# Kernel optimization log

Measured on AMD Instinct MI355X. Metric: run time of the kernel, lower is better.

The kernel has to match this reference:

```python
import jax, jax.numpy as jnp
import numpy as np

SEQ, H, VOCAB = 2048, 1024, 32000

def setup_inputs() -> dict:
    key = jax.random.key(0)
    ks = jax.random.split(key, 13)
    s = lambda k, shape, fan: jax.random.normal(k, shape, dtype=jnp.float32) / np.sqrt(fan)
    return {
        "word_input": jax.random.randint(ks[0], (1,), 0, VOCAB, dtype=jnp.int64),
        "last_context": s(ks[1], (1, H), H),
        "last_hidden": s(ks[2], (1, H), H),
        "encoder_outputs": s(ks[3], (SEQ, H), H),
        "emb": s(ks[4], (VOCAB, H), H),
        "W_ih": s(ks[5], (4 * H, 2 * H), 2 * H),
        "W_hh": s(ks[6], (4 * H, H), H),
        "b_ih": s(ks[7], (4 * H,), H),
        "b_hh": s(ks[8], (4 * H,), H),
        "Wa": s(ks[9], (H, H), H),
        "ba": s(ks[10], (H,), H),
        "Wl": s(ks[11], (VOCAB, 2 * H), 2 * H),
        "bl": s(ks[12], (VOCAB,), 2 * H),
    }

def reference(word_input, last_context, last_hidden, encoder_outputs,
              emb, W_ih, W_hh, b_ih, b_hh, Wa, ba, Wl, bl):
    # embedding lookup (batch=1, single step): [H]
    x = emb[word_input[0]]
    # rnn_input = cat(embedded, last_context): [2H]
    inp = jnp.concatenate([x, last_context[0]])
    h0 = last_hidden[0]
    c0 = jnp.zeros_like(h0)
    # single LSTM step, PyTorch gate order (i, f, g, o)
    gates = W_ih @ inp + b_ih + W_hh @ h0 + b_hh  # [4H]
    i_g, f_g, g_g, o_g = jnp.split(gates, 4)
    c = jax.nn.sigmoid(f_g) * c0 + jax.nn.sigmoid(i_g) * jnp.tanh(g_g)
    h = jax.nn.sigmoid(o_g) * jnp.tanh(c)  # lstm_output, [H]
    # Bahdanau-style scores: dot(h, Wa @ enc_i + ba) for each position (vectorized)
    energies = (encoder_outputs @ Wa.T + ba) @ h  # [SEQ]
    attn_w = jax.nn.softmax(energies)
    context = attn_w @ encoder_outputs  # [H]
    logits = Wl @ jnp.concatenate([h, context]) + bl  # [VOCAB]
    out = jax.nn.log_softmax(logits)
    return out[None, :]  # [1, VOCAB]
```

## Files before the change

### kernel.cpp

```cpp
#include <hip/hip_runtime.h>
#include <hip/hip_bf16.h>
#include <math.h>

#define SEQ   2048
#define H     1024
#define VOCAB 32000
#define GRID2 2048
#define NTHR  256

__device__ inline float4 ld4(const float* p) { return *reinterpret_cast<const float4*>(p); }
__device__ inline float dot4(float4 a, float4 b) { return a.x*b.x + a.y*b.y + a.z*b.z + a.w*b.w; }
__device__ inline float sigmoidf(float x) { return 1.f / (1.f + expf(-x)); }

__device__ inline void omerge(float& m, float& s, float m2, float s2) {
    if (m2 > m) { s = s * __expf(m - m2) + s2; m = m2; }
    else if (s2 != 0.f) { s += s2 * __expf(m2 - m); }
}
__device__ inline float waveSum(float v) {
#pragma unroll
    for (int off = 32; off > 0; off >>= 1) v += __shfl_down(v, off, 64);
    return v;
}
__device__ inline void waveOmerge(float& m, float& s) {
#pragma unroll
    for (int off = 32; off > 0; off >>= 1) {
        float m2 = __shfl_down(m, off, 64), ss = __shfl_down(s, off, 64);
        omerge(m, s, m2, ss);
    }
}

__device__ inline void blockSignal(unsigned* f) {
    __syncthreads();
    if (threadIdx.x == 0) {
        __threadfence();
        __hip_atomic_fetch_add(f, 1u, __ATOMIC_RELEASE, __HIP_MEMORY_SCOPE_AGENT);
    }
}
__device__ inline void blockWait(unsigned* f, unsigned target) {
    if (threadIdx.x == 0) {
        while (__hip_atomic_load(f, __ATOMIC_ACQUIRE, __HIP_MEMORY_SCOPE_AGENT) < target)
            __builtin_amdgcn_s_sleep(4);
        __threadfence();
    }
    __syncthreads();
}


__global__ __launch_bounds__(NTHR) void k_init(float* __restrict__ ws) {
    const int t = threadIdx.x;
    unsigned* fl = (unsigned*)ws;
    if (t < 96) fl[t] = 0u;
    float* u   = ws + 2144;
    float* ctx = ws + 1120;
    for (int k = t; k < H; k += NTHR) { u[k] = 0.f; ctx[k] = 0.f; }
}

__global__ __launch_bounds__(NTHR, 8) void k_main(
        const float* __restrict__ emb,  const float* __restrict__ lctx,
        const float* __restrict__ h0,   const float* __restrict__ W_ih,
        const float* __restrict__ W_hh, const float* __restrict__ b_ih,
        const float* __restrict__ b_hh, const int* __restrict__ widx,
        const float* __restrict__ enc,  const float* __restrict__ Wa,
        const float* __restrict__ Wl,   const float* __restrict__ bl,
        float* __restrict__ ws, float* __restrict__ out) {
    const int bid = blockIdx.x, t = threadIdx.x;
    const int wid = t >> 6, lane = t & 63;

    unsigned* f_h   = (unsigned*)ws + 0;
    unsigned* f_u   = (unsigned*)ws + 16;
    unsigned* f_e   = (unsigned*)ws + 32;
    unsigned* f_ctx = (unsigned*)ws + 48;
    unsigned* f_l   = (unsigned*)ws + 64;
    float*  h      = ws + 96;
    float*  ctx    = ws + 1120;
    float*  u      = ws + 2144;
    float*  energ  = ws + 3168;
    float2* part_e = (float2*)(ws + 5216);
    float2* part_l = (float2*)(ws + 5728);

    __shared__ float  lg[12];
    __shared__ float  shh[16];
    __shared__ float  se[8];
    __shared__ float  shw[32];
    __shared__ float2 s2[4];

    if (bid >= 1024) {
        const int j = bid - 1024;
        const int w = widx[0];
        const float* xe = emb + (size_t)w * H;
        const float* wi = W_ih + (size_t)j * (2 * H);
        const float* wg = W_ih + (size_t)(j + 2 * H) * (2 * H);
        const float* wo = W_ih + (size_t)(j + 3 * H) * (2 * H);
        const float* vi = W_hh + (size_t)j * H;
        const float* vg = W_hh + (size_t)(j + 2 * H) * H;
        const float* vo = W_hh + (size_t)(j + 3 * H) * H;
        const int e = t * 4;
        float4 x0 = ld4(xe + e), x1 = ld4(lctx + e), x2 = ld4(h0 + e);
        float ai = dot4(ld4(wi + e), x0) + dot4(ld4(wi + H + e), x1) + dot4(ld4(vi + e), x2);
        float ag = dot4(ld4(wg + e), x0) + dot4(ld4(wg + H + e), x1) + dot4(ld4(vg + e), x2);
        float ao = dot4(ld4(wo + e), x0) + dot4(ld4(wo + H + e), x1) + dot4(ld4(vo + e), x2);
        ai = waveSum(ai); ag = waveSum(ag); ao = waveSum(ao);
        if (lane == 0) { lg[wid*3] = ai; lg[wid*3+1] = ag; lg[wid*3+2] = ao; }
        __syncthreads();
        if (t == 0) {
            float gi = 0.f, gg = 0.f, go = 0.f;
            for (int q = 0; q < 4; ++q) { gi += lg[q*3]; gg += lg[q*3+1]; go += lg[q*3+2]; }
            gi += b_ih[j] + b_hh[j];
            gg += b_ih[j + 2*H] + b_hh[j + 2*H];
            go += b_ih[j + 3*H] + b_hh[j + 3*H];
            float c = sigmoidf(gi) * tanhf(gg);
            h[j] = sigmoidf(go) * tanhf(c);
        }
        blockSignal(f_h);
    }

    blockWait(f_h, 1024);

    if (bid < 256) {
        {
            const int rg = bid >> 2, kb = bid & 3;
            if (t < 16) shh[t] = h[rg * 16 + t];
            __syncthreads();
            const int k = kb * 256 + t;
            float acc = 0.f;
#pragma unroll
            for (int jj = 0; jj < 16; ++jj)
                acc += Wa[(size_t)(rg * 16 + jj) * H + k] * shh[jj];
            atomicAdd(&u[k], acc);
            blockSignal(f_u);
            blockWait(f_u, 256);
        }
        {
#pragma unroll
            for (int rr = 0; rr < 2; ++rr) {
                const int row = bid * 8 + wid * 2 + rr;
                const float* er = enc + (size_t)row * H;
                float acc = 0.f;
#pragma unroll
                for (int it = 0; it < 4; ++it) {
                    const int e = it * 256 + lane * 4;
                    acc += dot4(ld4(er + e), ld4(u + e));
                }
                acc = waveSum(acc);
                if (lane == 0) { energ[row] = acc; se[wid * 2 + rr] = acc; }
            }
            __syncthreads();
            if (t == 0) {
                float m = -INFINITY, s = 0.f;
                for (int q = 0; q < 8; ++q) omerge(m, s, se[q], 1.f);
                part_e[bid] = make_float2(m, s);
            }
            blockSignal(f_e);
            blockWait(f_e, 256);
        }
        {
            float2 p = part_e[t];
            float m = p.x, s = p.y;
            waveOmerge(m, s);
            if (lane == 0) s2[wid] = make_float2(m, s);
            __syncthreads();
            float M = s2[0].x, S = s2[0].y;
#pragma unroll
            for (int q = 1; q < 4; ++q) omerge(M, S, s2[q].x, s2[q].y);
            const float invS = 1.f / S;
            const int rg = bid >> 2, kb = bid & 3;
            __syncthreads();
            if (t < 32) shw[t] = __expf(energ[rg * 32 + t] - M) * invS;
            __syncthreads();
            const int k = kb * 256 + t;
            float acc = 0.f;
#pragma unroll
            for (int jj = 0; jj < 32; ++jj)
                acc += shw[jj] * enc[(size_t)(rg * 32 + jj) * H + k];
            atomicAdd(&ctx[k], acc);
            blockSignal(f_ctx);
        }
        if (bid < 125) {
            blockWait(f_l, 1792);
            float m = -INFINITY, s = 0.f;
            for (int i = t; i < 1792; i += NTHR) {
                float2 p = part_l[i];
                omerge(m, s, p.x, p.y);
            }
            waveOmerge(m, s);
            __syncthreads();
            if (lane == 0) s2[wid] = make_float2(m, s);
            __syncthreads();
            float M = s2[0].x, S = s2[0].y;
#pragma unroll
            for (int q = 1; q < 4; ++q) omerge(M, S, s2[q].x, s2[q].y);
            const float lse = M + logf(S);
            const int i = bid * 256 + t;
            out[i] = out[i] - lse;
        }
    } else {
        const int gwS = (bid - 256) * 4 + wid;
        const int NR = (gwS < 3328) ? 5 : 4;
        float4 xv[4];
#pragma unroll
        for (int q = 0; q < 4; ++q) xv[q] = ld4(h + q * 256 + lane * 4);
        float acc[5] = {0.f, 0.f, 0.f, 0.f, 0.f};
#pragma unroll
        for (int rr = 0; rr < 5; ++rr) {
            if (rr < NR) {
                const float* wr = Wl + (size_t)(gwS + 7168 * rr) * (2 * H);
                float a = 0.f;
#pragma unroll
                for (int q = 0; q < 4; ++q)
                    a += dot4(ld4(wr + q * 256 + lane * 4), xv[q]);
                acc[rr] = a;
            }
        }
        blockWait(f_ctx, 256);
#pragma unroll
        for (int q = 0; q < 4; ++q) xv[q] = ld4(ctx + q * 256 + lane * 4);
        float lm = -INFINITY, ls = 0.f;
#pragma unroll
        for (int rr = 0; rr < 5; ++rr) {
            if (rr < NR) {
                const int r = gwS + 7168 * rr;
                const float* wr = Wl + (size_t)r * (2 * H) + H;
                float a = acc[rr];
#pragma unroll
                for (int q = 0; q < 4; ++q)
                    a += dot4(ld4(wr + q * 256 + lane * 4), xv[q]);
                a = waveSum(a);
                if (lane == 0) {
                    float v = a + bl[r];
                    out[r] = v;
                    omerge(lm, ls, v, 1.f);
                }
            }
        }
        if (lane == 0) s2[wid] = make_float2(lm, ls);
        __syncthreads();
        if (t == 0) {
            float M = s2[0].x, S = s2[0].y;
#pragma unroll
            for (int q = 1; q < 4; ++q) omerge(M, S, s2[q].x, s2[q].y);
            part_l[bid - 256] = make_float2(M, S);
        }
        blockSignal(f_l);
    }
}


__global__ __launch_bounds__(256) void k_lstm(
        const float* __restrict__ emb, const float* __restrict__ lctx,
        const float* __restrict__ h0,  const float* __restrict__ W_ih,
        const float* __restrict__ W_hh, const float* __restrict__ b_ih,
        const float* __restrict__ b_hh, const int* __restrict__ widx,
        float* __restrict__ h_out, float* __restrict__ u_zero,
        float* __restrict__ ctx_zero) {
    const int j = blockIdx.x, t = threadIdx.x;
    const int wid = t >> 6, lane = t & 63;
    if (j == 0) for (int k = t; k < H; k += 256) u_zero[k] = 0.f;
    if (j == 1) for (int k = t; k < H; k += 256) ctx_zero[k] = 0.f;
    const int w = widx[0];
    const float* embrow = emb + (size_t)w * H;
    const int ri = j, rg = j + 2 * H, ro = j + 3 * H;
    const float* wi_i = W_ih + (size_t)ri * (2 * H);
    const float* wi_g = W_ih + (size_t)rg * (2 * H);
    const float* wi_o = W_ih + (size_t)ro * (2 * H);
    const float* wh_i = W_hh + (size_t)ri * H;
    const float* wh_g = W_hh + (size_t)rg * H;
    const float* wh_o = W_hh + (size_t)ro * H;
    float ai = 0.f, ag = 0.f, ao = 0.f;
    { int e = t*4; float4 x = ld4(embrow+e);
      ai += dot4(ld4(wi_i+e),x); ag += dot4(ld4(wi_g+e),x); ao += dot4(ld4(wi_o+e),x); }
    { int e = t*4; float4 x = ld4(lctx+e);
      ai += dot4(ld4(wi_i+H+e),x); ag += dot4(ld4(wi_g+H+e),x); ao += dot4(ld4(wi_o+H+e),x); }
    { int e = t*4; float4 x = ld4(h0+e);
      ai += dot4(ld4(wh_i+e),x); ag += dot4(ld4(wh_g+e),x); ao += dot4(ld4(wh_o+e),x); }
    ai = waveSum(ai); ag = waveSum(ag); ao = waveSum(ao);
    __shared__ float lds[12];
    if (lane == 0) { lds[wid*3] = ai; lds[wid*3+1] = ag; lds[wid*3+2] = ao; }
    __syncthreads();
    if (t == 0) {
        float gi = 0.f, gg = 0.f, go = 0.f;
        for (int q = 0; q < 4; ++q) { gi += lds[q*3]; gg += lds[q*3+1]; go += lds[q*3+2]; }
        gi += b_ih[ri] + b_hh[ri];
        gg += b_ih[rg] + b_hh[rg];
        go += b_ih[ro] + b_hh[ro];
        float c = sigmoidf(gi) * tanhf(gg);
        h_out[j] = sigmoidf(go) * tanhf(c);
    }
}

__global__ __launch_bounds__(256) void k_wa(
        const float* __restrict__ Wa, const float* __restrict__ h,
        float* __restrict__ u) {
    const int k = blockIdx.x * 256 + threadIdx.x;
    const int j0 = blockIdx.y * 32;
    float acc = 0.f;
#pragma unroll 8
    for (int j = j0; j < j0 + 32; ++j) acc += Wa[(size_t)j * H + k] * h[j];
    atomicAdd(&u[k], acc);
}

__global__ __launch_bounds__(256) void k_energy(
        const float* __restrict__ enc, const float* __restrict__ u,
        float* __restrict__ energ, float2* __restrict__ part_e) {
    const int t = threadIdx.x, wid = t >> 6, lane = t & 63;
    const int row = blockIdx.x * 4 + wid;
    const float* er = enc + (size_t)row * H;
    float acc = 0.f;
#pragma unroll
    for (int it = 0; it < 4; ++it) { int e = it*256 + lane*4; acc += dot4(ld4(er+e), ld4(u+e)); }
    acc = waveSum(acc);
    __shared__ float se[4];
    if (lane == 0) { energ[row] = acc; se[wid] = acc; }
    __syncthreads();
    if (t == 0) {
        float m = fmaxf(fmaxf(se[0], se[1]), fmaxf(se[2], se[3]));
        float s = __expf(se[0]-m) + __expf(se[1]-m) + __expf(se[2]-m) + __expf(se[3]-m);
        part_e[blockIdx.x] = make_float2(m, s);
    }
}

__global__ __launch_bounds__(256) void k_ctx(
        const float* __restrict__ enc, const float* __restrict__ energ,
        const float2* __restrict__ part_e, float* __restrict__ ctx) {
    const int t = threadIdx.x, wid = t >> 6, lane = t & 63;
    __shared__ float2 s2[4];
    __shared__ float sh[64];
    float2 a = part_e[t], b = part_e[t + 256];
    float m = a.x, s = a.y;
    omerge(m, s, b.x, b.y);
    waveOmerge(m, s);
    if (lane == 0) s2[wid] = make_float2(m, s);
    __syncthreads();
    float M = s2[0].x, S = s2[0].y;
#pragma unroll
    for (int q = 1; q < 4; ++q) omerge(M, S, s2[q].x, s2[q].y);
    const float invS = 1.f / S;
    const int j0 = (blockIdx.x >> 2) * 64;
    __syncthreads();
    if (t < 64) sh[t] = __expf(energ[j0 + t] - M) * invS;
    __syncthreads();
    const int k = (blockIdx.x & 3) * 256 + t;
    float acc = 0.f;
#pragma unroll 8
    for (int jj = 0; jj < 64; ++jj) acc += sh[jj] * enc[(size_t)(j0 + jj) * H + k];
    atomicAdd(&ctx[k], acc);
}

__global__ __launch_bounds__(256) void k_logits(
        const float* __restrict__ Wl, const float* __restrict__ vcat,
        const float* __restrict__ bl, float* __restrict__ logits,
        float2* __restrict__ part_l) {
    const int t = threadIdx.x, wid = t >> 6, lane = t & 63;
    const int gw = blockIdx.x * 4 + wid;
    float4 xv[8];
#pragma unroll
    for (int q = 0; q < 8; ++q) xv[q] = ld4(vcat + q * 256 + lane * 4);
    float lm = -INFINITY, ls = 0.f;
#pragma unroll
    for (int rr = 0; rr < 4; ++rr) {
        const int row = gw * 4 + rr;
        const float* wr = Wl + (size_t)row * (2 * H);
        float acc = 0.f;
#pragma unroll
        for (int q = 0; q < 8; ++q)
            acc += dot4(ld4(wr + q * 256 + lane * 4), xv[q]);
        acc = waveSum(acc);
        if (lane == 0) {
            float v = acc + bl[row];
            logits[row] = v;
            omerge(lm, ls, v, 1.f);
        }
    }
    __shared__ float2 s2[4];
    if (lane == 0) s2[wid] = make_float2(lm, ls);
    __syncthreads();
    if (t == 0) {
        float M = s2[0].x, S = s2[0].y;
#pragma unroll
        for (int q = 1; q < 4; ++q) omerge(M, S, s2[q].x, s2[q].y);
        part_l[blockIdx.x] = make_float2(M, S);
    }
}

__global__ __launch_bounds__(256) void k_final(
        const float* __restrict__ logits, const float2* __restrict__ part_l,
        float* __restrict__ out) {
    const int t = threadIdx.x, wid = t >> 6, lane = t & 63;
    __shared__ float2 s2[4];
    float m = -INFINITY, s = 0.f;
    for (int i = t; i < 2000; i += 256) {
        float2 p = part_l[i];
        omerge(m, s, p.x, p.y);
    }
    waveOmerge(m, s);
    if (lane == 0) s2[wid] = make_float2(m, s);
    __syncthreads();
    float M = s2[0].x, S = s2[0].y;
#pragma unroll
    for (int q = 1; q < 4; ++q) omerge(M, S, s2[q].x, s2[q].y);
    const float lse = M + logf(S);
    const int i = blockIdx.x * 256 + t;
    out[i] = logits[i] - lse;
}

extern "C" void kernel_launch(void* const* d_in, const int* in_sizes, int n_in,
                              void* d_out, int out_size, void* d_ws, size_t ws_size,
                              hipStream_t stream) {
    const int*   widx = (const int*)d_in[0];
    const float* lctx = (const float*)d_in[1];
    const float* h0   = (const float*)d_in[2];
    const float* enc  = (const float*)d_in[3];
    const float* emb  = (const float*)d_in[4];
    const float* W_ih = (const float*)d_in[5];
    const float* W_hh = (const float*)d_in[6];
    const float* b_ih = (const float*)d_in[7];
    const float* b_hh = (const float*)d_in[8];
    const float* Wa   = (const float*)d_in[9];
    const float* Wl   = (const float*)d_in[11];
    const float* bl   = (const float*)d_in[12];
    float* out = (float*)d_out;
    float* ws  = (float*)d_ws;

    int occ = 0, nCU = 0, dev = 0;
    hipGetDevice(&dev);
    hipDeviceGetAttribute(&nCU, hipDeviceAttributeMultiprocessorCount, dev);
    hipError_t oe = hipOccupancyMaxActiveBlocksPerMultiprocessor(
        &occ, (const void*)k_main, NTHR, 0);
    const bool persistent_ok = (oe == hipSuccess) && ((long)occ * nCU >= GRID2);

    if (persistent_ok) {
        k_init<<<1, NTHR, 0, stream>>>(ws);
        k_main<<<GRID2, NTHR, 0, stream>>>(emb, lctx, h0, W_ih, W_hh, b_ih,
                                           b_hh, widx, enc, Wa, Wl, bl, ws, out);
    } else {
        float*  h      = ws;
        float*  ctx    = ws + 1024;
        float*  u      = ws + 2048;
        float*  energ  = ws + 3072;
        float2* part_e = (float2*)(ws + 5120);
        float2* part_l = (float2*)(ws + 6144);
        float*  logits = ws + 10240;
        k_lstm  <<<1024, 256, 0, stream>>>(emb, lctx, h0, W_ih, W_hh, b_ih, b_hh, widx, h, u, ctx);
        k_wa    <<<dim3(4, 32), 256, 0, stream>>>(Wa, h, u);
        k_energy<<<512, 256, 0, stream>>>(enc, u, energ, part_e);
        k_ctx   <<<128, 256, 0, stream>>>(enc, energ, part_e, ctx);
        k_logits<<<2000, 256, 0, stream>>>(Wl, ws , bl, logits, part_l);
        k_final <<<125, 256, 0, stream>>>(logits, part_l, out);
    }
}
```

Baseline: 72.98 us.

## Rebalance fused decoder blocks: LSTM blocks also do logits, attention blocks take tail rows

```diff
diff --git a/kernel.cpp b/kernel.cpp
--- a/kernel.cpp
+++ b/kernel.cpp
@@ -9,6 +9,11 @@
 #define NTHR  256
 
 __device__ inline float4 ld4(const float* p) { return *reinterpret_cast<const float4*>(p); }
+typedef float vfloat4 __attribute__((ext_vector_type(4)));
+__device__ inline float4 ld4nt(const float* p) {
+    vfloat4 v = __builtin_nontemporal_load(reinterpret_cast<const vfloat4*>(p));
+    return make_float4(v.x, v.y, v.z, v.w);
+}
 __device__ inline float dot4(float4 a, float4 b) { return a.x*b.x + a.y*b.y + a.z*b.z + a.w*b.w; }
 __device__ inline float sigmoidf(float x) { return 1.f / (1.f + expf(-x)); }
 
@@ -49,9 +54,9 @@
 __global__ __launch_bounds__(NTHR) void k_init(float* __restrict__ ws) {
     const int t = threadIdx.x;
     unsigned* fl = (unsigned*)ws;
-    if (t < 96) fl[t] = 0u;
-    float* u   = ws + 2144;
-    float* ctx = ws + 1120;
+    if (t < 128) fl[t] = 0u;
+    float* ctx = ws + 1152;
+    float* u   = ws + 2176;
     for (int k = t; k < H; k += NTHR) { u[k] = 0.f; ctx[k] = 0.f; }
 }
 
@@ -71,12 +76,13 @@
     unsigned* f_e   = (unsigned*)ws + 32;
     unsigned* f_ctx = (unsigned*)ws + 48;
     unsigned* f_l   = (unsigned*)ws + 64;
-    float*  h      = ws + 96;
-    float*  ctx    = ws + 1120;
-    float*  u      = ws + 2144;
-    float*  energ  = ws + 3168;
-    float2* part_e = (float2*)(ws + 5216);
-    float2* part_l = (float2*)(ws + 5728);
+    float*  vcat   = ws + 128;
+    float*  h      = vcat;
+    float*  ctx    = vcat + H;
+    float*  u      = ws + 2176;
+    float*  energ  = ws + 3200;
+    float2* part_e = (float2*)(ws + 5248);
+    float2* part_l = (float2*)(ws + 5760);
 
     __shared__ float  lg[12];
     __shared__ float  shh[16];
@@ -84,10 +90,10 @@
     __shared__ float  shw[32];
     __shared__ float2 s2[4];
 
-    if (bid >= 1024) {
-        const int j = bid - 1024;
+    if (bid < 1024) {
+        const int j = bid;
         const int w = widx[0];
-        const float* xe = emb + (size_t)w * H;
+        const float* xep = emb + (size_t)w * H;
         const float* wi = W_ih + (size_t)j * (2 * H);
         const float* wg = W_ih + (size_t)(j + 2 * H) * (2 * H);
         const float* wo = W_ih + (size_t)(j + 3 * H) * (2 * H);
@@ -95,10 +101,10 @@
         const float* vg = W_hh + (size_t)(j + 2 * H) * H;
         const float* vo = W_hh + (size_t)(j + 3 * H) * H;
         const int e = t * 4;
-        float4 x0 = ld4(xe + e), x1 = ld4(lctx + e), x2 = ld4(h0 + e);
-        float ai = dot4(ld4(wi + e), x0) + dot4(ld4(wi + H + e), x1) + dot4(ld4(vi + e), x2);
-        float ag = dot4(ld4(wg + e), x0) + dot4(ld4(wg + H + e), x1) + dot4(ld4(vg + e), x2);
-        float ao = dot4(ld4(wo + e), x0) + dot4(ld4(wo + H + e), x1) + dot4(ld4(vo + e), x2);
+        float4 x0 = ld4(xep + e), x1 = ld4(lctx + e), x2 = ld4(h0 + e);
+        float ai = dot4(ld4nt(wi + e), x0) + dot4(ld4nt(wi + H + e), x1) + dot4(ld4nt(vi + e), x2);
+        float ag = dot4(ld4nt(wg + e), x0) + dot4(ld4nt(wg + H + e), x1) + dot4(ld4nt(vg + e), x2);
+        float ao = dot4(ld4nt(wo + e), x0) + dot4(ld4nt(wo + H + e), x1) + dot4(ld4nt(vo + e), x2);
         ai = waveSum(ai); ag = waveSum(ag); ao = waveSum(ao);
         if (lane == 0) { lg[wid*3] = ai; lg[wid*3+1] = ag; lg[wid*3+2] = ao; }
         __syncthreads();
@@ -116,9 +122,10 @@
 
     blockWait(f_h, 1024);
 
-    if (bid < 256) {
+    if (bid >= 1024 && bid < 1280) {
+        const int ab = bid - 1024;
         {
-            const int rg = bid >> 2, kb = bid & 3;
+            const int rg = ab >> 2, kb = ab & 3;
             if (t < 16) shh[t] = h[rg * 16 + t];
             __syncthreads();
             const int k = kb * 256 + t;
@@ -133,7 +140,7 @@
         {
 #pragma unroll
             for (int rr = 0; rr < 2; ++rr) {
-                const int row = bid * 8 + wid * 2 + rr;
+                const int row = ab * 8 + wid * 2 + rr;
                 const float* er = enc + (size_t)row * H;
                 float acc = 0.f;
 #pragma unroll
@@ -148,7 +155,7 @@
             if (t == 0) {
                 float m = -INFINITY, s = 0.f;
                 for (int q = 0; q < 8; ++q) omerge(m, s, se[q], 1.f);
-                part_e[bid] = make_float2(m, s);
+                part_e[ab] = make_float2(m, s);
             }
             blockSignal(f_e);
             blockWait(f_e, 256);
@@ -163,7 +170,7 @@
 #pragma unroll
             for (int q = 1; q < 4; ++q) omerge(M, S, s2[q].x, s2[q].y);
             const float invS = 1.f / S;
-            const int rg = bid >> 2, kb = bid & 3;
+            const int rg = ab >> 2, kb = ab & 3;
             __syncthreads();
             if (t < 32) shw[t] = __expf(energ[rg * 32 + t] - M) * invS;
             __syncthreads();
@@ -174,62 +181,74 @@
                 acc += shw[jj] * enc[(size_t)(rg * 32 + jj) * H + k];
             atomicAdd(&ctx[k], acc);
             blockSignal(f_ctx);
-        }
-        if (bid < 125) {
-            blockWait(f_l, 1792);
-            float m = -INFINITY, s = 0.f;
-            for (int i = t; i < 1792; i += NTHR) {
-                float2 p = part_l[i];
-                omerge(m, s, p.x, p.y);
+            blockWait(f_ctx, 256);
+        }
+        {
+            const int aw = ab * 4 + wid;
+            float4 xv[8];
+#pragma unroll
+            for (int q = 0; q < 8; ++q) xv[q] = ld4(vcat + q * 256 + lane * 4);
+            float lm = -INFINITY, ls = 0.f;
+#pragma unroll
+            for (int rr = 0; rr < 4; ++rr) {
+                if (rr < 3 || aw < 256) {
+                    const int r = 28672 + aw + 1024 * rr;
+                    const float* wr = Wl + (size_t)r * (2 * H);
+                    float a = 0.f;
+#pragma unroll
+                    for (int q = 0; q < 8; ++q)
+                        a += dot4(ld4(wr + q * 256 + lane * 4), xv[q]);
+                    a = waveSum(a);
+                    if (lane == 0) {
+                        float v = a + bl[r];
+                        out[r] = v;
+                        omerge(lm, ls, v, 1.f);
+                    }
+                }
             }
-            waveOmerge(m, s);
-            __syncthreads();
-            if (lane == 0) s2[wid] = make_float2(m, s);
-            __syncthreads();
-            float M = s2[0].x, S = s2[0].y;
-#pragma unroll
-            for (int q = 1; q < 4; ++q) omerge(M, S, s2[q].x, s2[q].y);
-            const float lse = M + logf(S);
-            const int i = bid * 256 + t;
-            out[i] = out[i] - lse;
+            if (lane == 0) s2[wid] = make_float2(lm, ls);
+            __syncthreads();
+            if (t == 0) {
+                float M = s2[0].x, S = s2[0].y;
+#pragma unroll
+                for (int q = 1; q < 4; ++q) omerge(M, S, s2[q].x, s2[q].y);
+                part_l[bid] = make_float2(M, S);
+            }
+            blockSignal(f_l);
         }
     } else {
-        const int gwS = (bid - 256) * 4 + wid;
-        const int NR = (gwS < 3328) ? 5 : 4;
+        const int sw = (bid < 1024) ? bid * 4 + wid : (bid - 256) * 4 + wid;
+        const int r0 = sw * 4;
         float4 xv[4];
 #pragma unroll
         for (int q = 0; q < 4; ++q) xv[q] = ld4(h + q * 256 + lane * 4);
-        float acc[5] = {0.f, 0.f, 0.f, 0.f, 0.f};
-#pragma unroll
-        for (int rr = 0; rr < 5; ++rr) {
-            if (rr < NR) {
-                const float* wr = Wl + (size_t)(gwS + 7168 * rr) * (2 * H);
-                float a = 0.f;
-#pragma unroll
-                for (int q = 0; q < 4; ++q)
-                    a += dot4(ld4(wr + q * 256 + lane * 4), xv[q]);
-                acc[rr] = a;
-            }
+        float acc4[4];
+#pragma unroll
+        for (int rr = 0; rr < 4; ++rr) {
+            const float* wr = Wl + (size_t)(r0 + rr) * (2 * H);
+            float a = 0.f;
+#pragma unroll
+            for (int q = 0; q < 4; ++q)
+                a += dot4(ld4(wr + q * 256 + lane * 4), xv[q]);
+            acc4[rr] = a;
         }
         blockWait(f_ctx, 256);
 #pragma unroll
         for (int q = 0; q < 4; ++q) xv[q] = ld4(ctx + q * 256 + lane * 4);
         float lm = -INFINITY, ls = 0.f;
 #pragma unroll
-        for (int rr = 0; rr < 5; ++rr) {
-            if (rr < NR) {
-                const int r = gwS + 7168 * rr;
-                const float* wr = Wl + (size_t)r * (2 * H) + H;
-                float a = acc[rr];
-#pragma unroll
-                for (int q = 0; q < 4; ++q)
-                    a += dot4(ld4(wr + q * 256 + lane * 4), xv[q]);
-                a = waveSum(a);
-                if (lane == 0) {
-                    float v = a + bl[r];
-                    out[r] = v;
-                    omerge(lm, ls, v, 1.f);
-                }
+        for (int rr = 0; rr < 4; ++rr) {
+            const int r = r0 + rr;
+            const float* wr = Wl + (size_t)r * (2 * H) + H;
+            float a = acc4[rr];
+#pragma unroll
+            for (int q = 0; q < 4; ++q)
+                a += dot4(ld4(wr + q * 256 + lane * 4), xv[q]);
+            a = waveSum(a);
+            if (lane == 0) {
+                float v = a + bl[r];
+                out[r] = v;
+                omerge(lm, ls, v, 1.f);
             }
         }
         if (lane == 0) s2[wid] = make_float2(lm, ls);
@@ -238,9 +257,28 @@
             float M = s2[0].x, S = s2[0].y;
 #pragma unroll
             for (int q = 1; q < 4; ++q) omerge(M, S, s2[q].x, s2[q].y);
-            part_l[bid - 256] = make_float2(M, S);
+            part_l[bid] = make_float2(M, S);
         }
         blockSignal(f_l);
+    }
+
+    if (bid < 125) {
+        blockWait(f_l, 2048);
+        float m = -INFINITY, s = 0.f;
+#pragma unroll
+        for (int q = 0; q < 8; ++q) {
+            float2 p = part_l[t + q * 256];
+            omerge(m, s, p.x, p.y);
+        }
+        waveOmerge(m, s);
+        if (lane == 0) s2[wid] = make_float2(m, s);
+        __syncthreads();
+        float M = s2[0].x, S = s2[0].y;
+#pragma unroll
+        for (int q = 1; q < 4; ++q) omerge(M, S, s2[q].x, s2[q].y);
+        const float lse = M + logf(S);
+        const int i = bid * 256 + t;
+        out[i] = out[i] - lse;
     }
 }
 
```

After: 74.47 us. 2.0% more time.
